# Performance work log

Measured on AMD Instinct MI355X. Metric: run time of the kernel, lower is better.

## Reference

```python
import jax, jax.numpy as jnp
import numpy as np


def setup_inputs() -> dict:
    key = jax.random.key(0)
    k1, k2, k3 = jax.random.split(key, 3)
    b, n, d, f = 16, 2048, 256, 256
    features = jax.random.normal(k1, (b, n, d), dtype=jnp.float32)
    # dense adjacency; row-normalize like MeanAggregator's normalized A
    A = jax.random.uniform(k2, (b, n, n), dtype=jnp.float32)
    A = A / jnp.sum(A, axis=-1, keepdims=True)
    weight = jax.random.normal(k3, (2 * d, f), dtype=jnp.float32) * (1.0 / np.sqrt(2 * d))
    bias = jnp.zeros((f,), dtype=jnp.float32)
    return {"features": features, "A": A, "weight": weight, "bias": bias}


def reference(features, A, weight, bias):
    # agg = A @ features  (MeanAggregator: row-normalized adjacency)
    agg = jnp.einsum('bnm,bmd->bnd', A, features)  # [b,n,d]
    d = features.shape[-1]
    # split-weight GEMM instead of materializing concat:
    # [feat, agg] @ W == feat @ W[:d] + agg @ W[d:]
    out = (jnp.einsum('bnd,df->bnf', features, weight[:d])
           + jnp.einsum('bnd,df->bnf', agg, weight[d:])
           + bias)
    return jax.nn.relu(out)
```

## Files before the change

### kernel.cpp

```cpp
#include <hip/hip_runtime.h>

typedef __attribute__((ext_vector_type(8))) short bf16x8;
typedef __attribute__((ext_vector_type(4))) float f32x4;

__device__ __forceinline__ unsigned short f2bf(float f) {
    unsigned int u = __builtin_bit_cast(unsigned int, f);
    unsigned int r = (u + 0x7FFFu + ((u >> 16) & 1u)) >> 16;
    return (unsigned short)r;
}
__device__ __forceinline__ unsigned int pkbf(float lo, float hi) {
    unsigned int ul = __builtin_bit_cast(unsigned int, lo) + 0x8000u;
    unsigned int uh = __builtin_bit_cast(unsigned int, hi) + 0x8000u;
    return (uh & 0xFFFF0000u) | (ul >> 16);
}
__device__ __forceinline__ float bf2f(unsigned short u) {
    unsigned int x = ((unsigned int)u) << 16;
    return __builtin_bit_cast(float, x);
}

__device__ __forceinline__ void gll16(const void* g, void* l) {
    __builtin_amdgcn_global_load_lds(
        (const __attribute__((address_space(1))) void*)g,
        (__attribute__((address_space(3))) void*)l, 16, 0, 0);
}

__global__ __launch_bounds__(256) void transpose_cvt_kernel(
    const float* __restrict__ src, unsigned short* __restrict__ dstT,
    unsigned short* __restrict__ dstS, int R, int C)
{
    __shared__ float tile[64][65];
    const int b = blockIdx.z;
    const float* s = src + (size_t)b * R * C;
    const int r0 = blockIdx.x * 64, c0 = blockIdx.y * 64;
    const int t = threadIdx.x;
    const int r = t >> 2, cg = (t & 3) * 16;

    float v[16];
    const float4* p = reinterpret_cast<const float4*>(s + (size_t)(r0 + r) * C + c0 + cg);
#pragma unroll
    for (int i = 0; i < 4; ++i) {
        float4 q = p[i];
        v[4 * i + 0] = q.x; v[4 * i + 1] = q.y; v[4 * i + 2] = q.z; v[4 * i + 3] = q.w;
    }
#pragma unroll
    for (int i = 0; i < 16; ++i) tile[r][cg + i] = v[i];

    if (dstS) {
        unsigned int w[8];
#pragma unroll
        for (int i = 0; i < 8; ++i)
            w[i] = (unsigned)f2bf(v[2 * i]) | ((unsigned)f2bf(v[2 * i + 1]) << 16);
        unsigned int* d = reinterpret_cast<unsigned int*>(
            dstS + (size_t)b * R * C + (size_t)(r0 + r) * C + c0 + cg);
        *reinterpret_cast<uint4*>(d)     = make_uint4(w[0], w[1], w[2], w[3]);
        *reinterpret_cast<uint4*>(d + 4) = make_uint4(w[4], w[5], w[6], w[7]);
    }

    __syncthreads();

    const int cl = t >> 2, rg = (t & 3) * 16;
    unsigned int w[8];
#pragma unroll
    for (int i = 0; i < 8; ++i) {
        unsigned short lo = f2bf(tile[rg + 2 * i][cl]);
        unsigned short hi = f2bf(tile[rg + 2 * i + 1][cl]);
        w[i] = (unsigned)lo | ((unsigned)hi << 16);
    }
    unsigned int* d = reinterpret_cast<unsigned int*>(
        dstT + (size_t)b * R * C + (size_t)(c0 + cl) * R + r0 + rg);
    *reinterpret_cast<uint4*>(d)     = make_uint4(w[0], w[1], w[2], w[3]);
    *reinterpret_cast<uint4*>(d + 4) = make_uint4(w[4], w[5], w[6], w[7]);
}

__global__ __launch_bounds__(256, 2) void kpre_gemm(
    const float* __restrict__ F, const unsigned short* __restrict__ Wt,
    const float* __restrict__ bias, unsigned short* __restrict__ H,
    unsigned short* __restrict__ Gt)
{
    __shared__ __align__(16) short Fb[64 * 256];
    __shared__ __align__(16) short Wb[256 * 64];

    const int tid = threadIdx.x;
    const int lane = tid & 63, wid = tid >> 6;
    const int lo = lane & 15, hi = lane >> 4;
    const int rb = blockIdx.x;
    const int batch = rb >> 5;
    const int mb = (rb & 31) * 64;
    const size_t m0g = (size_t)rb * 64;

    {
        const int frow = tid >> 2, fq = tid & 3;
        const float* fp = F + (m0g + frow) * 256 + fq * 64;
#pragma unroll
        for (int g = 0; g < 2; ++g) {
            float4 q[8];
#pragma unroll
            for (int i = 0; i < 8; ++i)
                q[i] = reinterpret_cast<const float4*>(fp)[g * 8 + i];
#pragma unroll
            for (int j = 0; j < 4; ++j) {
                unsigned int w0 = pkbf(q[2*j].x,   q[2*j].y);
                unsigned int w1 = pkbf(q[2*j].z,   q[2*j].w);
                unsigned int w2 = pkbf(q[2*j+1].x, q[2*j+1].y);
                unsigned int w3 = pkbf(q[2*j+1].z, q[2*j+1].w);
                int slot = fq * 8 + g * 4 + j;
                int off = frow * 256 + ((slot ^ (frow & 7)) << 3);
                *reinterpret_cast<uint4*>(&Fb[off]) = make_uint4(w0, w1, w2, w3);
            }
        }
    }

    f32x4 acc[4][4];

#pragma unroll
    for (int pass = 0; pass < 2; ++pass) {
#pragma unroll
        for (int m = 0; m < 4; ++m)
#pragma unroll
            for (int n = 0; n < 4; ++n) acc[m][n] = (f32x4){0.f, 0.f, 0.f, 0.f};

        for (int kt = 0; kt < 4; ++kt) {
            const int kbase = pass * 256 + kt * 64;
#pragma unroll
            for (int it = 0; it < 8; ++it) {
                int si = it * 256 + tid;
                int row = si >> 3, slot = si & 7;
                const unsigned short* g = Wt + (size_t)row * 512 + kbase + ((slot ^ (row & 7)) << 3);
                gll16(g, Wb + (size_t)si * 8);
            }
            __syncthreads();

#pragma unroll
            for (int kk = 0; kk < 2; ++kk) {
                bf16x8 af[4], bw[4];
#pragma unroll
                for (int m = 0; m < 4; ++m) {
                    int row = m * 16 + lo;
                    int slot = kt * 8 + kk * 4 + hi;
                    af[m] = *reinterpret_cast<const bf16x8*>(&Fb[row * 256 + ((slot ^ (row & 7)) << 3)]);
                }
#pragma unroll
                for (int n = 0; n < 4; ++n) {
                    int row = wid * 64 + n * 16 + lo;
                    bw[n] = *reinterpret_cast<const bf16x8*>(&Wb[row * 64 + (((kk * 4 + hi) ^ (row & 7)) << 3)]);
                }
#pragma unroll
                for (int m = 0; m < 4; ++m)
#pragma unroll
                    for (int n = 0; n < 4; ++n)
                        acc[m][n] = __builtin_amdgcn_mfma_f32_16x16x32_bf16(af[m], bw[n], acc[m][n], 0, 0, 0);
            }
            __syncthreads();
        }

        if (pass == 0) {
            float bv[4];
#pragma unroll
            for (int n = 0; n < 4; ++n) bv[n] = bias[wid * 64 + n * 16 + lo];
            unsigned short* Hb = H + m0g * 256;
#pragma unroll
            for (int m = 0; m < 4; ++m)
#pragma unroll
                for (int n = 0; n < 4; ++n)
#pragma unroll
                    for (int j = 0; j < 4; ++j) {
                        int row = m * 16 + hi * 4 + j;
                        int col = wid * 64 + n * 16 + lo;
                        Hb[(size_t)row * 256 + col] = f2bf(acc[m][n][j] + bv[n]);
                    }
        } else {
            short* T = Wb + wid * 4096;
#pragma unroll
            for (int m = 0; m < 4; ++m)
#pragma unroll
                for (int n = 0; n < 4; ++n)
#pragma unroll
                    for (int j = 0; j < 4; ++j) {
                        int gr = m * 16 + hi * 4 + j;
                        int gc = n * 16 + lo;
                        int slot = gr >> 3, e = gr & 7;
                        T[gc * 64 + ((slot ^ (gc & 7)) << 3) + e] = f2bf(acc[m][n][j]);
                    }
            unsigned short* Gb = Gt + ((size_t)batch * 256 + wid * 64) * 2048 + mb;
#pragma unroll
            for (int i = 0; i < 8; ++i) {
                int f = i * 8 + (lane >> 3);
                int s = lane & 7;
                bf16x8 v = *reinterpret_cast<const bf16x8*>(&T[f * 64 + ((s ^ (f & 7)) << 3)]);
                *reinterpret_cast<bf16x8*>(Gb + (size_t)f * 2048 + s * 8) = v;
            }
        }
    }
}

__global__ __launch_bounds__(512, 2) void kmain_gemm(
    const float* __restrict__ A, const unsigned short* __restrict__ Gt,
    const unsigned short* __restrict__ H, float* __restrict__ out)
{
    __shared__ __align__(16) short Ab[128 * 64];
    __shared__ __align__(16) short Bb[256 * 64];

    const int tid = threadIdx.x;
    const int lane = tid & 63, wid = tid >> 6;
    const int wr = wid >> 2, wc = wid & 3;
    const int lo = lane & 15, hi = lane >> 4;

    const int bid = blockIdx.x;
    const int wg = ((bid & 7) << 5) | (bid >> 3);
    const int batch = wg >> 4;
    const int mt    = wg & 15;

    const float* Abase = A + ((size_t)batch * 2048 + (size_t)mt * 128) * 2048;
    const unsigned short* Gbase = Gt + (size_t)batch * 256 * 2048;

    const int arow = tid >> 2;
    const int acg  = tid & 3;

    f32x4 acc[4][4];
#pragma unroll
    for (int m = 0; m < 4; ++m)
#pragma unroll
        for (int n = 0; n < 4; ++n) acc[m][n] = (f32x4){0.f, 0.f, 0.f, 0.f};

    float4 qa[4];
    auto load_A = [&](int k0) {
        const float4* p = reinterpret_cast<const float4*>(
            Abase + (size_t)arow * 2048 + k0 + acg * 16);
#pragma unroll
        for (int i = 0; i < 4; ++i) qa[i] = p[i];
    };

    load_A(0);

    for (int t = 0; t < 32; ++t) {
        const int k0 = t * 64;
#pragma unroll
        for (int it = 0; it < 4; ++it) {
            int si = it * 512 + tid;
            int row = si >> 3, slot = si & 7;
            const unsigned short* g = Gbase + (size_t)row * 2048 + k0 + ((slot ^ (row & 7)) << 3);
            gll16(g, Bb + (size_t)si * 8);
        }
        {
            unsigned int w0 = pkbf(qa[0].x, qa[0].y), w1 = pkbf(qa[0].z, qa[0].w);
            unsigned int w2 = pkbf(qa[1].x, qa[1].y), w3 = pkbf(qa[1].z, qa[1].w);
            unsigned int w4 = pkbf(qa[2].x, qa[2].y), w5 = pkbf(qa[2].z, qa[2].w);
            unsigned int w6 = pkbf(qa[3].x, qa[3].y), w7 = pkbf(qa[3].z, qa[3].w);
            int slin = acg * 2;
            int off0 = arow * 64 + (((slin    ) ^ (arow & 7)) << 3);
            int off1 = arow * 64 + (((slin + 1) ^ (arow & 7)) << 3);
            *reinterpret_cast<uint4*>(&Ab[off0]) = make_uint4(w0, w1, w2, w3);
            *reinterpret_cast<uint4*>(&Ab[off1]) = make_uint4(w4, w5, w6, w7);
        }
        __syncthreads();

        if (t + 1 < 32) load_A((t + 1) * 64);

#pragma unroll
        for (int kk = 0; kk < 2; ++kk) {
            bf16x8 af[4], bfv[4];
#pragma unroll
            for (int m = 0; m < 4; ++m) {
                int row = wr * 64 + m * 16 + lo;
                af[m] = *reinterpret_cast<const bf16x8*>(&Ab[row * 64 + (((kk * 4 + hi) ^ (row & 7)) << 3)]);
            }
#pragma unroll
            for (int n = 0; n < 4; ++n) {
                int row = wc * 64 + n * 16 + lo;
                bfv[n] = *reinterpret_cast<const bf16x8*>(&Bb[row * 64 + (((kk * 4 + hi) ^ (row & 7)) << 3)]);
            }
#pragma unroll
            for (int m = 0; m < 4; ++m)
#pragma unroll
                for (int n = 0; n < 4; ++n)
                    acc[m][n] = __builtin_amdgcn_mfma_f32_16x16x32_bf16(af[m], bfv[n], acc[m][n], 0, 0, 0);
        }
        __syncthreads();
    }

    const size_t rowbase = (size_t)batch * 2048 + (size_t)mt * 128;
    const unsigned short* Hb = H + rowbase * 256;
    float* obase = out + rowbase * 256;
#pragma unroll
    for (int m = 0; m < 4; ++m) {
#pragma unroll
        for (int n = 0; n < 4; ++n) {
            int col = wc * 64 + n * 16 + lo;
#pragma unroll
            for (int j = 0; j < 4; ++j) {
                int row = wr * 64 + m * 16 + hi * 4 + j;
                float v = acc[m][n][j] + bf2f(Hb[(size_t)row * 256 + col]);
                obase[(size_t)row * 256 + col] = fmaxf(v, 0.f);
            }
        }
    }
}

extern "C" void kernel_launch(void* const* d_in, const int* in_sizes, int n_in,
                              void* d_out, int out_size, void* d_ws, size_t ws_size,
                              hipStream_t stream) {
    const float* features = (const float*)d_in[0];
    const float* A        = (const float*)d_in[1];
    const float* weight   = (const float*)d_in[2];
    const float* bias     = (const float*)d_in[3];
    float* out = (float*)d_out;

    const size_t WT_B = (size_t)256 * 512 * 2;
    const size_t H_B  = (size_t)32768 * 256 * 2;
    const size_t GT_B = (size_t)16 * 256 * 2048 * 2;
    if (ws_size < WT_B + H_B + GT_B) return;

    char* ws = (char*)d_ws;
    unsigned short* Wt = (unsigned short*)ws;
    unsigned short* H  = (unsigned short*)(ws + WT_B);
    unsigned short* Gt = (unsigned short*)(ws + WT_B + H_B);

    dim3 gW(512 / 64, 256 / 64, 1);
    transpose_cvt_kernel<<<gW, 256, 0, stream>>>(weight, Wt, nullptr, 512, 256);

    kpre_gemm<<<512, 256, 0, stream>>>(features, Wt, bias, H, Gt);

    kmain_gemm<<<256, 512, 0, stream>>>(A, Gt, H, out);
}
```

Before: 115.4 us.

## Double-buffer LDS tiles with manual waitcnt pipelining in the main GEMM

Allocates two LDS buffers for the A and B tiles and restructures the K loop so the next tile's global-to-LDS B loads and A register loads are issued while MFMAs run on the current buffer. The per-step barriers are replaced by explicit s_waitcnt vmcnt(4)/lgkmcnt(0) plus s_barrier, so only the older loads are waited on. MFMA blocks are wrapped in s_setprio to favour the math wave. This doubles LDS use to about 96KB per block, which may stop two blocks from sharing a CU, and it depends on the hand-counted vmcnt values being right.

```diff
diff --git a/kernel.cpp b/kernel.cpp
--- a/kernel.cpp
+++ b/kernel.cpp
@@ -197,8 +197,8 @@
     const float* __restrict__ A, const unsigned short* __restrict__ Gt,
     const unsigned short* __restrict__ H, float* __restrict__ out)
 {
-    __shared__ __align__(16) short Ab[128 * 64];
-    __shared__ __align__(16) short Bb[256 * 64];
+    __shared__ __align__(16) short Ab[2][128 * 64];
+    __shared__ __align__(16) short Bb[2][256 * 64];
 
     const int tid = threadIdx.x;
     const int lane = tid & 63, wid = tid >> 6;
@@ -222,61 +222,92 @@
 #pragma unroll
         for (int n = 0; n < 4; ++n) acc[m][n] = (f32x4){0.f, 0.f, 0.f, 0.f};
 
-    float4 qa[4];
-    auto load_A = [&](int k0) {
+    float4 qa0[4], qa1[4];
+
+    auto loadA = [&](float4* q, int k0) {
         const float4* p = reinterpret_cast<const float4*>(
             Abase + (size_t)arow * 2048 + k0 + acg * 16);
 #pragma unroll
-        for (int i = 0; i < 4; ++i) qa[i] = p[i];
+        for (int i = 0; i < 4; ++i) q[i] = p[i];
     };
-
-    load_A(0);
-
-    for (int t = 0; t < 32; ++t) {
-        const int k0 = t * 64;
+    auto writeA = [&](int buf, const float4* q) {
+        unsigned int w0 = pkbf(q[0].x, q[0].y), w1 = pkbf(q[0].z, q[0].w);
+        unsigned int w2 = pkbf(q[1].x, q[1].y), w3 = pkbf(q[1].z, q[1].w);
+        unsigned int w4 = pkbf(q[2].x, q[2].y), w5 = pkbf(q[2].z, q[2].w);
+        unsigned int w6 = pkbf(q[3].x, q[3].y), w7 = pkbf(q[3].z, q[3].w);
+        int slin = acg * 2;
+        int off0 = arow * 64 + (((slin    ) ^ (arow & 7)) << 3);
+        int off1 = arow * 64 + (((slin + 1) ^ (arow & 7)) << 3);
+        *reinterpret_cast<uint4*>(&Ab[buf][off0]) = make_uint4(w0, w1, w2, w3);
+        *reinterpret_cast<uint4*>(&Ab[buf][off1]) = make_uint4(w4, w5, w6, w7);
+    };
+    auto stageB = [&](int buf, int k0) {
 #pragma unroll
         for (int it = 0; it < 4; ++it) {
             int si = it * 512 + tid;
             int row = si >> 3, slot = si & 7;
             const unsigned short* g = Gbase + (size_t)row * 2048 + k0 + ((slot ^ (row & 7)) << 3);
-            gll16(g, Bb + (size_t)si * 8);
-        }
-        {
-            unsigned int w0 = pkbf(qa[0].x, qa[0].y), w1 = pkbf(qa[0].z, qa[0].w);
-            unsigned int w2 = pkbf(qa[1].x, qa[1].y), w3 = pkbf(qa[1].z, qa[1].w);
-            unsigned int w4 = pkbf(qa[2].x, qa[2].y), w5 = pkbf(qa[2].z, qa[2].w);
-            unsigned int w6 = pkbf(qa[3].x, qa[3].y), w7 = pkbf(qa[3].z, qa[3].w);
-            int slin = acg * 2;
-            int off0 = arow * 64 + (((slin    ) ^ (arow & 7)) << 3);
-            int off1 = arow * 64 + (((slin + 1) ^ (arow & 7)) << 3);
-            *reinterpret_cast<uint4*>(&Ab[off0]) = make_uint4(w0, w1, w2, w3);
-            *reinterpret_cast<uint4*>(&Ab[off1]) = make_uint4(w4, w5, w6, w7);
-        }
-        __syncthreads();
-
-        if (t + 1 < 32) load_A((t + 1) * 64);
-
+            gll16(g, &Bb[buf][(size_t)si * 8]);
+        }
+    };
+    auto compute = [&](int buf) {
 #pragma unroll
         for (int kk = 0; kk < 2; ++kk) {
             bf16x8 af[4], bfv[4];
 #pragma unroll
             for (int m = 0; m < 4; ++m) {
                 int row = wr * 64 + m * 16 + lo;
-                af[m] = *reinterpret_cast<const bf16x8*>(&Ab[row * 64 + (((kk * 4 + hi) ^ (row & 7)) << 3)]);
+                af[m] = *reinterpret_cast<const bf16x8*>(
+                    &Ab[buf][row * 64 + (((kk * 4 + hi) ^ (row & 7)) << 3)]);
             }
 #pragma unroll
             for (int n = 0; n < 4; ++n) {
                 int row = wc * 64 + n * 16 + lo;
-                bfv[n] = *reinterpret_cast<const bf16x8*>(&Bb[row * 64 + (((kk * 4 + hi) ^ (row & 7)) << 3)]);
-            }
+                bfv[n] = *reinterpret_cast<const bf16x8*>(
+                    &Bb[buf][row * 64 + (((kk * 4 + hi) ^ (row & 7)) << 3)]);
+            }
+            __builtin_amdgcn_s_setprio(1);
 #pragma unroll
             for (int m = 0; m < 4; ++m)
 #pragma unroll
                 for (int n = 0; n < 4; ++n)
                     acc[m][n] = __builtin_amdgcn_mfma_f32_16x16x32_bf16(af[m], bfv[n], acc[m][n], 0, 0, 0);
-        }
-        __syncthreads();
-    }
+            __builtin_amdgcn_s_setprio(0);
+        }
+    };
+
+    loadA(qa0, 0);
+    stageB(0, 0);
+    writeA(0, qa0);
+    loadA(qa1, 64);
+    asm volatile("s_waitcnt vmcnt(4) lgkmcnt(0)" ::: "memory");
+    __builtin_amdgcn_s_barrier();
+    asm volatile("" ::: "memory");
+    stageB(1, 64);
+
+    for (int tt = 0; tt < 15; ++tt) {
+        const int t0 = tt * 2;
+        writeA(1, qa1);
+        loadA(qa0, (t0 + 2) * 64);
+        compute(0);
+        asm volatile("s_waitcnt vmcnt(4) lgkmcnt(0)" ::: "memory");
+        __builtin_amdgcn_s_barrier();
+        asm volatile("" ::: "memory");
+        stageB(0, (t0 + 2) * 64);
+        writeA(0, qa0);
+        loadA(qa1, (t0 + 3) * 64);
+        compute(1);
+        asm volatile("s_waitcnt vmcnt(4) lgkmcnt(0)" ::: "memory");
+        __builtin_amdgcn_s_barrier();
+        asm volatile("" ::: "memory");
+        stageB(1, (t0 + 3) * 64);
+    }
+    writeA(1, qa1);
+    compute(0);
+    asm volatile("s_waitcnt vmcnt(0) lgkmcnt(0)" ::: "memory");
+    __builtin_amdgcn_s_barrier();
+    asm volatile("" ::: "memory");
+    compute(1);
 
     const size_t rowbase = (size_t)batch * 2048 + (size_t)mt * 128;
     const unsigned short* Hb = H + rowbase * 256;
```

Result: faster. 112.6 us (-2.4%).

## Pre-convert adjacency to bf16 and double-buffer main GEMM with async LDS loads

Applied to the files above, without the earlier changes.

Adds a separate pass that converts the fp32 adjacency matrix to bf16 in workspace. The main GEMM can then stage both A and G tiles with direct global-to-LDS loads into double buffers, instead of converting A in registers on the critical path. The output N dimension is split into two 128-wide tiles to double the block count, and MFMA sections get raised wave priority. In exchange it adds a full extra read of the fp32 A plus a bf16 write of it, and the bf16 A is now read by two blocks per row tile, which raises total memory traffic on a bandwidth-bound problem.

```diff
diff --git a/kernel.cpp b/kernel.cpp
--- a/kernel.cpp
+++ b/kernel.cpp
@@ -193,12 +193,33 @@
     }
 }
 
-__global__ __launch_bounds__(512, 2) void kmain_gemm(
-    const float* __restrict__ A, const unsigned short* __restrict__ Gt,
+__global__ __launch_bounds__(256) void kconv_A(
+    const float* __restrict__ A, unsigned short* __restrict__ Abf, long long n4)
+{
+    const long long tid = (long long)blockIdx.x * 256 + threadIdx.x;
+    const long long stride = (long long)gridDim.x * 256;
+    for (long long base = tid; base < n4; base += stride * 4) {
+        float4 q0, q1, q2, q3;
+        long long i0 = base, i1 = base + stride, i2 = base + 2 * stride, i3 = base + 3 * stride;
+        q0 = reinterpret_cast<const float4*>(A)[i0];
+        if (i1 < n4) q1 = reinterpret_cast<const float4*>(A)[i1];
+        if (i2 < n4) q2 = reinterpret_cast<const float4*>(A)[i2];
+        if (i3 < n4) q3 = reinterpret_cast<const float4*>(A)[i3];
+        uint2 w;
+        w.x = pkbf(q0.x, q0.y); w.y = pkbf(q0.z, q0.w);
+        reinterpret_cast<uint2*>(Abf)[i0] = w;
+        if (i1 < n4) { w.x = pkbf(q1.x, q1.y); w.y = pkbf(q1.z, q1.w); reinterpret_cast<uint2*>(Abf)[i1] = w; }
+        if (i2 < n4) { w.x = pkbf(q2.x, q2.y); w.y = pkbf(q2.z, q2.w); reinterpret_cast<uint2*>(Abf)[i2] = w; }
+        if (i3 < n4) { w.x = pkbf(q3.x, q3.y); w.y = pkbf(q3.z, q3.w); reinterpret_cast<uint2*>(Abf)[i3] = w; }
+    }
+}
+
+__global__ __launch_bounds__(512, 4) void kmain2_gemm(
+    const unsigned short* __restrict__ Abf, const unsigned short* __restrict__ Gt,
     const unsigned short* __restrict__ H, float* __restrict__ out)
 {
-    __shared__ __align__(16) short Ab[128 * 64];
-    __shared__ __align__(16) short Bb[256 * 64];
+    __shared__ __align__(16) short Ab[2][128 * 64];
+    __shared__ __align__(16) short Bb[2][128 * 64];
 
     const int tid = threadIdx.x;
     const int lane = tid & 63, wid = tid >> 6;
@@ -206,76 +227,70 @@
     const int lo = lane & 15, hi = lane >> 4;
 
     const int bid = blockIdx.x;
-    const int wg = ((bid & 7) << 5) | (bid >> 3);
-    const int batch = wg >> 4;
-    const int mt    = wg & 15;
-
-    const float* Abase = A + ((size_t)batch * 2048 + (size_t)mt * 128) * 2048;
-    const unsigned short* Gbase = Gt + (size_t)batch * 256 * 2048;
-
-    const int arow = tid >> 2;
-    const int acg  = tid & 3;
-
-    f32x4 acc[4][4];
+    const int wg = ((bid & 7) << 6) | (bid >> 3);
+    const int batch = wg >> 5;
+    const int mt    = (wg >> 1) & 15;
+    const int nt    = wg & 1;
+
+    const unsigned short* Abase = Abf + ((size_t)batch * 2048 + (size_t)mt * 128) * 2048;
+    const unsigned short* Gbase = Gt + ((size_t)batch * 256 + (size_t)nt * 128) * 2048;
+
+    f32x4 acc[4][2];
 #pragma unroll
     for (int m = 0; m < 4; ++m)
 #pragma unroll
-        for (int n = 0; n < 4; ++n) acc[m][n] = (f32x4){0.f, 0.f, 0.f, 0.f};
-
-    float4 qa[4];
-    auto load_A = [&](int k0) {
-        const float4* p = reinterpret_cast<const float4*>(
-            Abase + (size_t)arow * 2048 + k0 + acg * 16);
-#pragma unroll
-        for (int i = 0; i < 4; ++i) qa[i] = p[i];
-    };
-
-    load_A(0);
-
-    for (int t = 0; t < 32; ++t) {
-        const int k0 = t * 64;
-#pragma unroll
-        for (int it = 0; it < 4; ++it) {
+        for (int n = 0; n < 2; ++n) acc[m][n] = (f32x4){0.f, 0.f, 0.f, 0.f};
+
+    auto stage = [&](int buf, int k0) {
+#pragma unroll
+        for (int it = 0; it < 2; ++it) {
+            int si = it * 512 + tid;
+            int row = si >> 3, slot = si & 7;
+            const unsigned short* g = Abase + (size_t)row * 2048 + k0 + ((slot ^ (row & 7)) << 3);
+            gll16(g, &Ab[buf][(size_t)si * 8]);
+        }
+#pragma unroll
+        for (int it = 0; it < 2; ++it) {
             int si = it * 512 + tid;
             int row = si >> 3, slot = si & 7;
             const unsigned short* g = Gbase + (size_t)row * 2048 + k0 + ((slot ^ (row & 7)) << 3);
-            gll16(g, Bb + (size_t)si * 8);
-        }
-        {
-            unsigned int w0 = pkbf(qa[0].x, qa[0].y), w1 = pkbf(qa[0].z, qa[0].w);
-            unsigned int w2 = pkbf(qa[1].x, qa[1].y), w3 = pkbf(qa[1].z, qa[1].w);
-            unsigned int w4 = pkbf(qa[2].x, qa[2].y), w5 = pkbf(qa[2].z, qa[2].w);
-            unsigned int w6 = pkbf(qa[3].x, qa[3].y), w7 = pkbf(qa[3].z, qa[3].w);
-            int slin = acg * 2;
-            int off0 = arow * 64 + (((slin    ) ^ (arow & 7)) << 3);
-            int off1 = arow * 64 + (((slin + 1) ^ (arow & 7)) << 3);
-            *reinterpret_cast<uint4*>(&Ab[off0]) = make_uint4(w0, w1, w2, w3);
-            *reinterpret_cast<uint4*>(&Ab[off1]) = make_uint4(w4, w5, w6, w7);
-        }
-        __syncthreads();
-
-        if (t + 1 < 32) load_A((t + 1) * 64);
-
+            gll16(g, &Bb[buf][(size_t)si * 8]);
+        }
+    };
+    auto compute = [&](int buf) {
 #pragma unroll
         for (int kk = 0; kk < 2; ++kk) {
-            bf16x8 af[4], bfv[4];
+            bf16x8 af[4], bfv[2];
 #pragma unroll
             for (int m = 0; m < 4; ++m) {
                 int row = wr * 64 + m * 16 + lo;
-                af[m] = *reinterpret_cast<const bf16x8*>(&Ab[row * 64 + (((kk * 4 + hi) ^ (row & 7)) << 3)]);
-            }
-#pragma unroll
-            for (int n = 0; n < 4; ++n) {
-                int row = wc * 64 + n * 16 + lo;
-                bfv[n] = *reinterpret_cast<const bf16x8*>(&Bb[row * 64 + (((kk * 4 + hi) ^ (row & 7)) << 3)]);
-            }
+                af[m] = *reinterpret_cast<const bf16x8*>(
+                    &Ab[buf][row * 64 + (((kk * 4 + hi) ^ (row & 7)) << 3)]);
+            }
+#pragma unroll
+            for (int n = 0; n < 2; ++n) {
+                int row = wc * 32 + n * 16 + lo;
+                bfv[n] = *reinterpret_cast<const bf16x8*>(
+                    &Bb[buf][row * 64 + (((kk * 4 + hi) ^ (row & 7)) << 3)]);
+            }
+            __builtin_amdgcn_s_setprio(1);
 #pragma unroll
             for (int m = 0; m < 4; ++m)
 #pragma unroll
-                for (int n = 0; n < 4; ++n)
+                for (int n = 0; n < 2; ++n)
                     acc[m][n] = __builtin_amdgcn_mfma_f32_16x16x32_bf16(af[m], bfv[n], acc[m][n], 0, 0, 0);
-        }
+            __builtin_amdgcn_s_setprio(0);
+        }
+    };
+
+    stage(0, 0);
+    __syncthreads();
+    stage(1, 64);
+
+    for (int t = 0; t < 32; ++t) {
+        compute(t & 1);
         __syncthreads();
+        if (t + 2 < 32) stage(t & 1, (t + 2) * 64);
     }
 
     const size_t rowbase = (size_t)batch * 2048 + (size_t)mt * 128;
@@ -284,8 +299,8 @@
 #pragma unroll
     for (int m = 0; m < 4; ++m) {
 #pragma unroll
-        for (int n = 0; n < 4; ++n) {
-            int col = wc * 64 + n * 16 + lo;
+        for (int n = 0; n < 2; ++n) {
+            int col = nt * 128 + wc * 32 + n * 16 + lo;
 #pragma unroll
             for (int j = 0; j < 4; ++j) {
                 int row = wr * 64 + m * 16 + hi * 4 + j;
@@ -305,20 +320,25 @@
     const float* bias     = (const float*)d_in[3];
     float* out = (float*)d_out;
 
-    const size_t WT_B = (size_t)256 * 512 * 2;
-    const size_t H_B  = (size_t)32768 * 256 * 2;
-    const size_t GT_B = (size_t)16 * 256 * 2048 * 2;
-    if (ws_size < WT_B + H_B + GT_B) return;
+    const size_t WT_B  = (size_t)256 * 512 * 2;
+    const size_t H_B   = (size_t)32768 * 256 * 2;
+    const size_t GT_B  = (size_t)16 * 256 * 2048 * 2;
+    const size_t ABF_B = (size_t)16 * 2048 * 2048 * 2;
+    if (ws_size < WT_B + H_B + GT_B + ABF_B) return;
 
     char* ws = (char*)d_ws;
-    unsigned short* Wt = (unsigned short*)ws;
-    unsigned short* H  = (unsigned short*)(ws + WT_B);
-    unsigned short* Gt = (unsigned short*)(ws + WT_B + H_B);
+    unsigned short* Wt  = (unsigned short*)ws;
+    unsigned short* H   = (unsigned short*)(ws + WT_B);
+    unsigned short* Gt  = (unsigned short*)(ws + WT_B + H_B);
+    unsigned short* Abf = (unsigned short*)(ws + WT_B + H_B + GT_B);
 
     dim3 gW(512 / 64, 256 / 64, 1);
     transpose_cvt_kernel<<<gW, 256, 0, stream>>>(weight, Wt, nullptr, 512, 256);
 
     kpre_gemm<<<512, 256, 0, stream>>>(features, Wt, bias, H, Gt);
 
-    kmain_gemm<<<256, 512, 0, stream>>>(A, Gt, H, out);
-}
+    const long long n4 = (long long)16 * 2048 * 2048 / 4;
+    kconv_A<<<2048, 256, 0, stream>>>(A, Abf, n4);
+
+    kmain2_gemm<<<512, 512, 0, stream>>>(Abf, Gt, H, out);
+}
```

Result: slower. 175.7 us (+52.3%).

## Split-K main GEMM into two halves with bf16 partials and reduction kernel

Applied to the files above, without the earlier changes.

The main A@G GEMM moves from 256 blocks of 128x256 tiles to 1024 blocks of 64x256 tiles, with the K dimension split in two. Each block writes bf16 partial sums to a workspace, and a new elementwise kernel adds both partials plus H and applies ReLU. The loop is restructured to issue the next A load before compute, and MFMA priority is raised. The goal is more parallelism and occupancy, at the cost of an extra kernel launch, extra partial-sum traffic, and extra bf16 rounding of the partials.

```diff
diff --git a/kernel.cpp b/kernel.cpp
--- a/kernel.cpp
+++ b/kernel.cpp
@@ -193,28 +193,28 @@
     }
 }
 
-__global__ __launch_bounds__(512, 2) void kmain_gemm(
+__global__ __launch_bounds__(256, 4) void kmain_gemm(
     const float* __restrict__ A, const unsigned short* __restrict__ Gt,
-    const unsigned short* __restrict__ H, float* __restrict__ out)
+    unsigned short* __restrict__ P)
 {
-    __shared__ __align__(16) short Ab[128 * 64];
+    __shared__ __align__(16) short Ab[64 * 64];
     __shared__ __align__(16) short Bb[256 * 64];
 
     const int tid = threadIdx.x;
     const int lane = tid & 63, wid = tid >> 6;
-    const int wr = wid >> 2, wc = wid & 3;
     const int lo = lane & 15, hi = lane >> 4;
 
     const int bid = blockIdx.x;
-    const int wg = ((bid & 7) << 5) | (bid >> 3);
-    const int batch = wg >> 4;
-    const int mt    = wg & 15;
-
-    const float* Abase = A + ((size_t)batch * 2048 + (size_t)mt * 128) * 2048;
-    const unsigned short* Gbase = Gt + (size_t)batch * 256 * 2048;
+    const int wg = ((bid & 7) << 7) | (bid >> 3);
+    const int batch = wg >> 6;
+    const int ks    = (wg >> 5) & 1;
+    const int mt    = wg & 31;
+
+    const float* Abase = A + ((size_t)batch * 2048 + (size_t)mt * 64) * 2048 + ks * 1024;
+    const unsigned short* Gbase = Gt + (size_t)batch * 256 * 2048 + ks * 1024;
 
     const int arow = tid >> 2;
-    const int acg  = tid & 3;
+    const int aq   = tid & 3;
 
     f32x4 acc[4][4];
 #pragma unroll
@@ -223,76 +223,115 @@
         for (int n = 0; n < 4; ++n) acc[m][n] = (f32x4){0.f, 0.f, 0.f, 0.f};
 
     float4 qa[4];
-    auto load_A = [&](int k0) {
+    auto loadA = [&](int k0) {
         const float4* p = reinterpret_cast<const float4*>(
-            Abase + (size_t)arow * 2048 + k0 + acg * 16);
+            Abase + (size_t)arow * 2048 + k0 + aq * 16);
 #pragma unroll
         for (int i = 0; i < 4; ++i) qa[i] = p[i];
     };
-
-    load_A(0);
-
-    for (int t = 0; t < 32; ++t) {
-        const int k0 = t * 64;
-#pragma unroll
-        for (int it = 0; it < 4; ++it) {
-            int si = it * 512 + tid;
+    auto writeA = [&]() {
+#pragma unroll
+        for (int j = 0; j < 2; ++j) {
+            uint4 w;
+            w.x = pkbf(qa[2*j].x,   qa[2*j].y);
+            w.y = pkbf(qa[2*j].z,   qa[2*j].w);
+            w.z = pkbf(qa[2*j+1].x, qa[2*j+1].y);
+            w.w = pkbf(qa[2*j+1].z, qa[2*j+1].w);
+            int slin = aq * 2 + j;
+            int off = arow * 64 + ((slin ^ (arow & 7)) << 3);
+            *reinterpret_cast<uint4*>(&Ab[off]) = w;
+        }
+    };
+    auto stageB = [&](int k0) {
+#pragma unroll
+        for (int it = 0; it < 8; ++it) {
+            int si = it * 256 + tid;
             int row = si >> 3, slot = si & 7;
             const unsigned short* g = Gbase + (size_t)row * 2048 + k0 + ((slot ^ (row & 7)) << 3);
-            gll16(g, Bb + (size_t)si * 8);
-        }
-        {
-            unsigned int w0 = pkbf(qa[0].x, qa[0].y), w1 = pkbf(qa[0].z, qa[0].w);
-            unsigned int w2 = pkbf(qa[1].x, qa[1].y), w3 = pkbf(qa[1].z, qa[1].w);
-            unsigned int w4 = pkbf(qa[2].x, qa[2].y), w5 = pkbf(qa[2].z, qa[2].w);
-            unsigned int w6 = pkbf(qa[3].x, qa[3].y), w7 = pkbf(qa[3].z, qa[3].w);
-            int slin = acg * 2;
-            int off0 = arow * 64 + (((slin    ) ^ (arow & 7)) << 3);
-            int off1 = arow * 64 + (((slin + 1) ^ (arow & 7)) << 3);
-            *reinterpret_cast<uint4*>(&Ab[off0]) = make_uint4(w0, w1, w2, w3);
-            *reinterpret_cast<uint4*>(&Ab[off1]) = make_uint4(w4, w5, w6, w7);
-        }
-        __syncthreads();
-
-        if (t + 1 < 32) load_A((t + 1) * 64);
-
+            gll16(g, &Bb[(size_t)si * 8]);
+        }
+    };
+    auto compute = [&]() {
 #pragma unroll
         for (int kk = 0; kk < 2; ++kk) {
             bf16x8 af[4], bfv[4];
 #pragma unroll
             for (int m = 0; m < 4; ++m) {
-                int row = wr * 64 + m * 16 + lo;
-                af[m] = *reinterpret_cast<const bf16x8*>(&Ab[row * 64 + (((kk * 4 + hi) ^ (row & 7)) << 3)]);
+                int row = m * 16 + lo;
+                af[m] = *reinterpret_cast<const bf16x8*>(
+                    &Ab[row * 64 + (((kk * 4 + hi) ^ (row & 7)) << 3)]);
             }
 #pragma unroll
             for (int n = 0; n < 4; ++n) {
-                int row = wc * 64 + n * 16 + lo;
-                bfv[n] = *reinterpret_cast<const bf16x8*>(&Bb[row * 64 + (((kk * 4 + hi) ^ (row & 7)) << 3)]);
-            }
+                int row = wid * 64 + n * 16 + lo;
+                bfv[n] = *reinterpret_cast<const bf16x8*>(
+                    &Bb[row * 64 + (((kk * 4 + hi) ^ (row & 7)) << 3)]);
+            }
+            __builtin_amdgcn_s_setprio(1);
 #pragma unroll
             for (int m = 0; m < 4; ++m)
 #pragma unroll
                 for (int n = 0; n < 4; ++n)
                     acc[m][n] = __builtin_amdgcn_mfma_f32_16x16x32_bf16(af[m], bfv[n], acc[m][n], 0, 0, 0);
-        }
+            __builtin_amdgcn_s_setprio(0);
+        }
+    };
+
+    loadA(0);
+    stageB(0);
+    writeA();
+    __syncthreads();
+
+    for (int t = 0; t < 16; ++t) {
+        if (t + 1 < 16) loadA((t + 1) * 64);
+        compute();
         __syncthreads();
-    }
-
-    const size_t rowbase = (size_t)batch * 2048 + (size_t)mt * 128;
-    const unsigned short* Hb = H + rowbase * 256;
-    float* obase = out + rowbase * 256;
+        if (t + 1 < 16) {
+            stageB((t + 1) * 64);
+            writeA();
+            __syncthreads();
+        }
+    }
+
+    unsigned short* Pb = P + ((size_t)ks * 32768 + (size_t)batch * 2048 + (size_t)mt * 64) * 256;
 #pragma unroll
     for (int m = 0; m < 4; ++m) {
 #pragma unroll
         for (int n = 0; n < 4; ++n) {
-            int col = wc * 64 + n * 16 + lo;
+            int col = wid * 64 + n * 16 + lo;
 #pragma unroll
             for (int j = 0; j < 4; ++j) {
-                int row = wr * 64 + m * 16 + hi * 4 + j;
-                float v = acc[m][n][j] + bf2f(Hb[(size_t)row * 256 + col]);
-                obase[(size_t)row * 256 + col] = fmaxf(v, 0.f);
-            }
-        }
+                int row = m * 16 + hi * 4 + j;
+                Pb[(size_t)row * 256 + col] = f2bf(acc[m][n][j]);
+            }
+        }
+    }
+}
+
+__global__ __launch_bounds__(256) void kred_kernel(
+    const unsigned short* __restrict__ P, const unsigned short* __restrict__ H,
+    float* __restrict__ out)
+{
+    const long long n8 = (long long)32768 * 256 / 8;
+    const long long p1 = (long long)32768 * 256;
+    long long i = (long long)blockIdx.x * 256 + threadIdx.x;
+    const long long stride = (long long)gridDim.x * 256;
+    for (; i < n8; i += stride) {
+        bf16x8 a = *reinterpret_cast<const bf16x8*>(&P[i * 8]);
+        bf16x8 b = *reinterpret_cast<const bf16x8*>(&P[p1 + i * 8]);
+        bf16x8 h = *reinterpret_cast<const bf16x8*>(&H[i * 8]);
+        float4 o0, o1;
+        float v;
+        v = bf2f((unsigned short)a[0]) + bf2f((unsigned short)b[0]) + bf2f((unsigned short)h[0]); o0.x = fmaxf(v, 0.f);
+        v = bf2f((unsigned short)a[1]) + bf2f((unsigned short)b[1]) + bf2f((unsigned short)h[1]); o0.y = fmaxf(v, 0.f);
+        v = bf2f((unsigned short)a[2]) + bf2f((unsigned short)b[2]) + bf2f((unsigned short)h[2]); o0.z = fmaxf(v, 0.f);
+        v = bf2f((unsigned short)a[3]) + bf2f((unsigned short)b[3]) + bf2f((unsigned short)h[3]); o0.w = fmaxf(v, 0.f);
+        v = bf2f((unsigned short)a[4]) + bf2f((unsigned short)b[4]) + bf2f((unsigned short)h[4]); o1.x = fmaxf(v, 0.f);
+        v = bf2f((unsigned short)a[5]) + bf2f((unsigned short)b[5]) + bf2f((unsigned short)h[5]); o1.y = fmaxf(v, 0.f);
+        v = bf2f((unsigned short)a[6]) + bf2f((unsigned short)b[6]) + bf2f((unsigned short)h[6]); o1.z = fmaxf(v, 0.f);
+        v = bf2f((unsigned short)a[7]) + bf2f((unsigned short)b[7]) + bf2f((unsigned short)h[7]); o1.w = fmaxf(v, 0.f);
+        reinterpret_cast<float4*>(out + i * 8)[0] = o0;
+        reinterpret_cast<float4*>(out + i * 8)[1] = o1;
     }
 }
 
@@ -308,17 +347,21 @@
     const size_t WT_B = (size_t)256 * 512 * 2;
     const size_t H_B  = (size_t)32768 * 256 * 2;
     const size_t GT_B = (size_t)16 * 256 * 2048 * 2;
-    if (ws_size < WT_B + H_B + GT_B) return;
+    const size_t P_B  = (size_t)2 * 32768 * 256 * 2;
+    if (ws_size < WT_B + H_B + GT_B + P_B) return;
 
     char* ws = (char*)d_ws;
     unsigned short* Wt = (unsigned short*)ws;
     unsigned short* H  = (unsigned short*)(ws + WT_B);
     unsigned short* Gt = (unsigned short*)(ws + WT_B + H_B);
+    unsigned short* P  = (unsigned short*)(ws + WT_B + H_B + GT_B);
 
     dim3 gW(512 / 64, 256 / 64, 1);
     transpose_cvt_kernel<<<gW, 256, 0, stream>>>(weight, Wt, nullptr, 512, 256);
 
     kpre_gemm<<<512, 256, 0, stream>>>(features, Wt, bias, H, Gt);
 
-    kmain_gemm<<<256, 512, 0, stream>>>(A, Gt, H, out);
-}
+    kmain_gemm<<<1024, 256, 0, stream>>>(A, Gt, P);
+
+    kred_kernel<<<2048, 256, 0, stream>>>(P, H, out);
+}
```

Result: slower. 129.1 us (+11.9%).
